# Performance work log

Measured on AMD Instinct MI355X. Metric: run time of the kernel, lower is better.

## Reference

```python
import jax, jax.numpy as jnp
import numpy as np

MARGIN = 1.0
EPS = 1e-8  # torch F.cosine_similarity default eps


def setup_inputs() -> dict:
    key = jax.random.key(0)
    k1, k2 = jax.random.split(key)
    reps = jax.random.normal(k1, (8192, 512), dtype=jnp.float32)
    labels = jax.random.randint(k2, (8192,), 0, 100, dtype=jnp.int64)
    return {"reps": reps, "labels": labels}


def reference(reps, labels):
    # cosine_similarity(reps[None, :, :], reps[:, None, :], dim=2)
    # == dot(a,b) / (max(||a||,eps) * max(||b||,eps)); compute via normalize + GEMM
    norms = jnp.maximum(jnp.linalg.norm(reps, axis=1, keepdims=True), EPS)
    xn = reps / norms  # [N, D]
    cos_sim = xn @ xn.T  # [N, N]
    label_matrix = labels[None, :] == labels[:, None]  # [N, N] bool
    same_class_loss = jnp.where(label_matrix, (1.0 - cos_sim) ** 2, 0.0)
    diff_class_loss = jnp.where(label_matrix, 0.0,
                                jnp.maximum(MARGIN - cos_sim, 0.0) ** 2)
    loss = same_class_loss + diff_class_loss
    return loss.mean()
```

## Files before the change

kernel.cpp:

```cpp
#include <hip/hip_runtime.h>


typedef __attribute__((ext_vector_type(8))) short  s8;
typedef __attribute__((ext_vector_type(8))) __bf16 bf8;
typedef __attribute__((ext_vector_type(4))) float  f4;
typedef __attribute__((ext_vector_type(4))) unsigned short u4v;

#define NTILE 36
#define PS_F32 (NTILE * 4096)

#define OFF_XT  0u
#define OFF_INV (8u * 1024u * 1024u)
#define OFF_S   (OFF_INV + 8192u * 4u)
#define OFF_S2  (OFF_S + 512u * 4u)
#define OFF_GP  (8u * 1024u * 1024u + 65536u)

__device__ __forceinline__ unsigned short f2bf(float f) {
    union { float f; unsigned u; } v; v.f = f;
    unsigned r = v.u + 0x7FFFu + ((v.u >> 16) & 1u);
    return (unsigned short)(r >> 16);
}

__global__ __launch_bounds__(256) void k_norms(
    const float* __restrict__ reps, float* __restrict__ inv,
    float* __restrict__ zbuf )
{
    const int t = threadIdx.x, lane = t & 63, w = t >> 6;
    if (blockIdx.x == 0) {
        for (int z = t; z < 513; z += 256) zbuf[z] = 0.f;
    }
    const int row = blockIdx.x * 4 + w;
    const float4 x0 = *(const float4*)(reps + (size_t)row * 512 + lane * 4);
    const float4 x1 = *(const float4*)(reps + (size_t)row * 512 + 256 + lane * 4);
    float ss = x0.x*x0.x + x0.y*x0.y + x0.z*x0.z + x0.w*x0.w
             + x1.x*x1.x + x1.y*x1.y + x1.z*x1.z + x1.w*x1.w;
    #pragma unroll
    for (int off = 1; off < 64; off <<= 1) ss += __shfl_xor(ss, off, 64);
    if (lane == 0) inv[row] = 1.0f / fmaxf(sqrtf(ss), 1e-8f);
}

__global__ __launch_bounds__(256) void k_norm_transpose(
    const float* __restrict__ reps, const float* __restrict__ inv,
    unsigned short* __restrict__ xt, float* __restrict__ svec)
{
    __shared__ unsigned short tile[64][72];
    __shared__ float sred[4][64];
    const int t = threadIdx.x, lane = t & 63, w = t >> 6;
    const int a0 = blockIdx.x * 64, i0 = blockIdx.y * 64;
    const int colg = t & 15;
    const int ig0  = t >> 4;

    float4 sa = {0.f, 0.f, 0.f, 0.f};
    #pragma unroll
    for (int j = 0; j < 4; ++j) {
        const int il = ig0 + j * 16;
        const float iv = inv[i0 + il];
        const float4 x = *(const float4*)(reps + (size_t)(i0 + il) * 512 + a0 + colg * 4);
        const float4 xn = {x.x * iv, x.y * iv, x.z * iv, x.w * iv};
        sa.x += xn.x; sa.y += xn.y; sa.z += xn.z; sa.w += xn.w;
        ushort4 p;
        p.x = f2bf(xn.x); p.y = f2bf(xn.y); p.z = f2bf(xn.z); p.w = f2bf(xn.w);
        *(ushort4*)&tile[il][colg * 4] = p;
    }
    __syncthreads();

    {
        const int ig = t & 15, ag = t >> 4;
        u4v rows[4];
        #pragma unroll
        for (int r = 0; r < 4; ++r)
            rows[r] = *(const u4v*)&tile[ig * 4 + r][ag * 4];
        #pragma unroll
        for (int j = 0; j < 4; ++j) {
            ushort4 o;
            o.x = (unsigned short)rows[0][j];
            o.y = (unsigned short)rows[1][j];
            o.z = (unsigned short)rows[2][j];
            o.w = (unsigned short)rows[3][j];
            *(ushort4*)(xt + (size_t)(a0 + ag * 4 + j) * 8192 + i0 + ig * 4) = o;
        }
    }

    sa.x += __shfl_xor(sa.x, 16, 64); sa.x += __shfl_xor(sa.x, 32, 64);
    sa.y += __shfl_xor(sa.y, 16, 64); sa.y += __shfl_xor(sa.y, 32, 64);
    sa.z += __shfl_xor(sa.z, 16, 64); sa.z += __shfl_xor(sa.z, 32, 64);
    sa.w += __shfl_xor(sa.w, 16, 64); sa.w += __shfl_xor(sa.w, 32, 64);
    if (lane < 16) {
        sred[w][lane * 4 + 0] = sa.x; sred[w][lane * 4 + 1] = sa.y;
        sred[w][lane * 4 + 2] = sa.z; sred[w][lane * 4 + 3] = sa.w;
    }
    __syncthreads();
    if (t < 64) {
        const float v = sred[0][t] + sred[1][t] + sred[2][t] + sred[3][t];
        atomicAdd(&svec[a0 + t], v);
    }
}

__global__ __launch_bounds__(64) void k_gram(
    const unsigned short* __restrict__ xt, float* __restrict__ gp, int kc)
{
    const int lane = threadIdx.x;
    const int l15 = lane & 15, l4 = lane >> 4;
    int tt = blockIdx.x, ta = 0;
    while (tt >= 8 - ta) { tt -= 8 - ta; ++ta; }
    const int tb = ta + tt;
    const int a0 = ta * 64, b0 = tb * 64;
    const int k0 = blockIdx.z * kc;
    const unsigned short* Arow = xt + (size_t)(a0 + l15) * 8192;
    const unsigned short* Brow = xt + (size_t)(b0 + l15) * 8192;

    f4 acc[4][4];
    #pragma unroll
    for (int mi = 0; mi < 4; ++mi)
        #pragma unroll
        for (int ni = 0; ni < 4; ++ni) {
            f4 z = {0.f, 0.f, 0.f, 0.f};
            acc[mi][ni] = z;
        }

    for (int k = 0; k < kc; k += 32) {
        const int ko = k0 + k + l4 * 8;
        s8 af[4], bfr[4];
        #pragma unroll
        for (int mi = 0; mi < 4; ++mi)
            af[mi] = *(const s8*)(Arow + (size_t)mi * 16 * 8192 + ko);
        #pragma unroll
        for (int ni = 0; ni < 4; ++ni)
            bfr[ni] = *(const s8*)(Brow + (size_t)ni * 16 * 8192 + ko);
        #pragma unroll
        for (int mi = 0; mi < 4; ++mi)
            #pragma unroll
            for (int ni = 0; ni < 4; ++ni)
                acc[mi][ni] = __builtin_amdgcn_mfma_f32_16x16x32_bf16(
                    __builtin_bit_cast(bf8, af[mi]),
                    __builtin_bit_cast(bf8, bfr[ni]),
                    acc[mi][ni], 0, 0, 0);
    }

    float* gb = gp + (size_t)blockIdx.z * PS_F32 + (size_t)blockIdx.x * 4096;
    #pragma unroll
    for (int mi = 0; mi < 4; ++mi)
        #pragma unroll
        for (int ni = 0; ni < 4; ++ni)
            #pragma unroll
            for (int r = 0; r < 4; ++r) {
                const int a_ = mi * 16 + l4 * 4 + r;
                const int b_ = ni * 16 + l15;
                gb[a_ * 64 + b_] = acc[mi][ni][r];
            }
}

__global__ __launch_bounds__(256) void k_reduce(
    const float* __restrict__ gp, float* __restrict__ s2, int ksplit)
{
    const int c = blockIdx.x * 256 + threadIdx.x;
    const f4* g4 = (const f4*)gp;
    f4 s = {0.f, 0.f, 0.f, 0.f};
    for (int p = 0; p < ksplit; ++p) s += g4[(size_t)p * (PS_F32 / 4) + c];
    int tt = c >> 10, ta = 0;
    while (tt >= 8 - ta) { tt -= 8 - ta; ++ta; }
    const float wgt = (tt == 0) ? 1.f : 2.f;
    float sq = wgt * (s.x * s.x + s.y * s.y + s.z * s.z + s.w * s.w);
    #pragma unroll
    for (int off = 1; off < 64; off <<= 1) sq += __shfl_xor(sq, off, 64);
    __shared__ float part[4];
    if ((threadIdx.x & 63) == 0) part[threadIdx.x >> 6] = sq;
    __syncthreads();
    if (threadIdx.x == 0) atomicAdd(s2, part[0] + part[1] + part[2] + part[3]);
}

__global__ __launch_bounds__(512) void k_final(
    const float* __restrict__ svec, const float* __restrict__ s2,
    float* __restrict__ out)
{
    const int t = threadIdx.x;
    float v = svec[t];
    float p = v * v;
    #pragma unroll
    for (int off = 1; off < 64; off <<= 1) p += __shfl_xor(p, off, 64);
    __shared__ float part[8];
    if ((t & 63) == 0) part[t >> 6] = p;
    __syncthreads();
    if (t == 0) {
        float s1 = 0.f;
        #pragma unroll
        for (int q = 0; q < 8; ++q) s1 += part[q];
        const double NN = 67108864.0;
        double loss = (NN - 2.0 * (double)s1 + (double)(*s2)) / NN;
        out[0] = (float)loss;
    }
}

extern "C" void kernel_launch(void* const* d_in, const int* in_sizes, int n_in,
                              void* d_out, int out_size, void* d_ws, size_t ws_size,
                              hipStream_t stream)
{
    const float* reps = (const float*)d_in[0];
    char* ws = (char*)d_ws;
    unsigned short* xt   = (unsigned short*)(ws + OFF_XT);
    float*          invn = (float*)(ws + OFF_INV);
    float*          svec = (float*)(ws + OFF_S);
    float*          s2   = (float*)(ws + OFF_S2);
    float*          gp   = (float*)(ws + OFF_GP);

    const size_t psb = (size_t)PS_F32 * 4;
    int ksplit = 8;
    if (ws_size >= OFF_GP + 32 * psb)      ksplit = 32;
    else if (ws_size >= OFF_GP + 16 * psb) ksplit = 16;
    const int kc = 8192 / ksplit;

    k_norms<<<2048, 256, 0, stream>>>(reps, invn, svec);
    k_norm_transpose<<<dim3(8, 128), 256, 0, stream>>>(reps, invn, xt, svec);
    k_gram<<<dim3(NTILE, 1, ksplit), 64, 0, stream>>>(xt, gp, kc);
    k_reduce<<<144, 256, 0, stream>>>(gp, s2, ksplit);
    k_final<<<1, 512, 0, stream>>>(svec, s2, (float*)d_out);
}
```

Baseline: 97.45 us.

## Use 32x32 Gram tiles with fixed K-split and fuse reduce with final

The upper-triangle tiling of the 512x512 Gram matrix moves from 64x64 tiles (36 tiles) to 32x32 tiles (136 tiles), with a fixed split of K=8192 into 16 chunks. This gives more workgroups to fill the GPU's compute units and removes the workspace-size-dependent split. The separate final kernel is folded into the reduction kernel through an atomic ticket, so the last block computes the loss and one launch is saved. In exchange, each tile reuses its loaded operands less, fewer rows per block share each fragment load, and the ticket counter must be zeroed (it is added to the zeroing range).

```diff
diff --git a/kernel.cpp b/kernel.cpp
--- a/kernel.cpp
+++ b/kernel.cpp
@@ -6,14 +6,16 @@
 typedef __attribute__((ext_vector_type(4))) float  f4;
 typedef __attribute__((ext_vector_type(4))) unsigned short u4v;
 
-#define NTILE 36
-#define PS_F32 (NTILE * 4096)
+#define NT32 136
+#define KOUT 16
+#define KCW  512
 
 #define OFF_XT  0u
 #define OFF_INV (8u * 1024u * 1024u)
 #define OFF_S   (OFF_INV + 8192u * 4u)
 #define OFF_S2  (OFF_S + 512u * 4u)
-#define OFF_GP  (8u * 1024u * 1024u + 65536u)
+#define OFF_TK  (OFF_S2 + 4u)
+#define OFF_GP  (OFF_S2 + 64u)
 
 __device__ __forceinline__ unsigned short f2bf(float f) {
     union { float f; unsigned u; } v; v.f = f;
@@ -27,7 +29,7 @@
 {
     const int t = threadIdx.x, lane = t & 63, w = t >> 6;
     if (blockIdx.x == 0) {
-        for (int z = t; z < 513; z += 256) zbuf[z] = 0.f;
+        for (int z = t; z < 514; z += 256) zbuf[z] = 0.f;
     }
     const int row = blockIdx.x * 4 + w;
     const float4 x0 = *(const float4*)(reps + (size_t)row * 512 + lane * 4);
@@ -97,97 +99,97 @@
 }
 
 __global__ __launch_bounds__(64) void k_gram(
-    const unsigned short* __restrict__ xt, float* __restrict__ gp, int kc)
+    const unsigned short* __restrict__ xt, float* __restrict__ gp)
 {
     const int lane = threadIdx.x;
     const int l15 = lane & 15, l4 = lane >> 4;
     int tt = blockIdx.x, ta = 0;
-    while (tt >= 8 - ta) { tt -= 8 - ta; ++ta; }
+    while (tt >= 16 - ta) { tt -= 16 - ta; ++ta; }
     const int tb = ta + tt;
-    const int a0 = ta * 64, b0 = tb * 64;
-    const int k0 = blockIdx.z * kc;
-    const unsigned short* Arow = xt + (size_t)(a0 + l15) * 8192;
-    const unsigned short* Brow = xt + (size_t)(b0 + l15) * 8192;
-
-    f4 acc[4][4];
-    #pragma unroll
-    for (int mi = 0; mi < 4; ++mi)
-        #pragma unroll
-        for (int ni = 0; ni < 4; ++ni) {
+    const int k0 = blockIdx.y * KCW;
+    const unsigned short* Arow = xt + (size_t)(ta * 32 + l15) * 8192;
+    const unsigned short* Brow = xt + (size_t)(tb * 32 + l15) * 8192;
+
+    f4 acc[2][2];
+    #pragma unroll
+    for (int mi = 0; mi < 2; ++mi)
+        #pragma unroll
+        for (int ni = 0; ni < 2; ++ni) {
             f4 z = {0.f, 0.f, 0.f, 0.f};
             acc[mi][ni] = z;
         }
 
-    for (int k = 0; k < kc; k += 32) {
+    for (int k = 0; k < KCW; k += 32) {
         const int ko = k0 + k + l4 * 8;
-        s8 af[4], bfr[4];
-        #pragma unroll
-        for (int mi = 0; mi < 4; ++mi)
-            af[mi] = *(const s8*)(Arow + (size_t)mi * 16 * 8192 + ko);
-        #pragma unroll
-        for (int ni = 0; ni < 4; ++ni)
-            bfr[ni] = *(const s8*)(Brow + (size_t)ni * 16 * 8192 + ko);
-        #pragma unroll
-        for (int mi = 0; mi < 4; ++mi)
+        s8 af[2], bfr[2];
+        af[0]  = *(const s8*)(Arow + ko);
+        af[1]  = *(const s8*)(Arow + (size_t)16 * 8192 + ko);
+        bfr[0] = *(const s8*)(Brow + ko);
+        bfr[1] = *(const s8*)(Brow + (size_t)16 * 8192 + ko);
+        #pragma unroll
+        for (int mi = 0; mi < 2; ++mi)
             #pragma unroll
-            for (int ni = 0; ni < 4; ++ni)
+            for (int ni = 0; ni < 2; ++ni)
                 acc[mi][ni] = __builtin_amdgcn_mfma_f32_16x16x32_bf16(
                     __builtin_bit_cast(bf8, af[mi]),
                     __builtin_bit_cast(bf8, bfr[ni]),
                     acc[mi][ni], 0, 0, 0);
     }
 
-    float* gb = gp + (size_t)blockIdx.z * PS_F32 + (size_t)blockIdx.x * 4096;
-    #pragma unroll
-    for (int mi = 0; mi < 4; ++mi)
-        #pragma unroll
-        for (int ni = 0; ni < 4; ++ni)
+    float* gb = gp + ((size_t)blockIdx.y * NT32 + blockIdx.x) * 1024;
+    #pragma unroll
+    for (int mi = 0; mi < 2; ++mi)
+        #pragma unroll
+        for (int ni = 0; ni < 2; ++ni)
             #pragma unroll
             for (int r = 0; r < 4; ++r) {
                 const int a_ = mi * 16 + l4 * 4 + r;
                 const int b_ = ni * 16 + l15;
-                gb[a_ * 64 + b_] = acc[mi][ni][r];
+                gb[a_ * 32 + b_] = acc[mi][ni][r];
             }
 }
 
-__global__ __launch_bounds__(256) void k_reduce(
-    const float* __restrict__ gp, float* __restrict__ s2, int ksplit)
-{
-    const int c = blockIdx.x * 256 + threadIdx.x;
+__global__ __launch_bounds__(256) void k_reduce_final(
+    const float* __restrict__ gp, const float* __restrict__ svec,
+    float* __restrict__ s2, int* __restrict__ ticket,
+    float* __restrict__ out)
+{
+    __shared__ float part[4];
+    __shared__ int lastFlag;
+    const int t = threadIdx.x;
+    const int c = blockIdx.x * 256 + t;
     const f4* g4 = (const f4*)gp;
     f4 s = {0.f, 0.f, 0.f, 0.f};
-    for (int p = 0; p < ksplit; ++p) s += g4[(size_t)p * (PS_F32 / 4) + c];
-    int tt = c >> 10, ta = 0;
-    while (tt >= 8 - ta) { tt -= 8 - ta; ++ta; }
+    #pragma unroll
+    for (int p = 0; p < KOUT; ++p) s += g4[(size_t)p * (NT32 * 256) + c];
+    int tt = c >> 8, ta = 0;
+    while (tt >= 16 - ta) { tt -= 16 - ta; ++ta; }
     const float wgt = (tt == 0) ? 1.f : 2.f;
     float sq = wgt * (s.x * s.x + s.y * s.y + s.z * s.z + s.w * s.w);
     #pragma unroll
     for (int off = 1; off < 64; off <<= 1) sq += __shfl_xor(sq, off, 64);
-    __shared__ float part[4];
-    if ((threadIdx.x & 63) == 0) part[threadIdx.x >> 6] = sq;
-    __syncthreads();
-    if (threadIdx.x == 0) atomicAdd(s2, part[0] + part[1] + part[2] + part[3]);
-}
-
-__global__ __launch_bounds__(512) void k_final(
-    const float* __restrict__ svec, const float* __restrict__ s2,
-    float* __restrict__ out)
-{
-    const int t = threadIdx.x;
-    float v = svec[t];
-    float p = v * v;
-    #pragma unroll
-    for (int off = 1; off < 64; off <<= 1) p += __shfl_xor(p, off, 64);
-    __shared__ float part[8];
-    if ((t & 63) == 0) part[t >> 6] = p;
+    if ((t & 63) == 0) part[t >> 6] = sq;
     __syncthreads();
     if (t == 0) {
-        float s1 = 0.f;
-        #pragma unroll
-        for (int q = 0; q < 8; ++q) s1 += part[q];
-        const double NN = 67108864.0;
-        double loss = (NN - 2.0 * (double)s1 + (double)(*s2)) / NN;
-        out[0] = (float)loss;
+        atomicAdd(s2, part[0] + part[1] + part[2] + part[3]);
+        __threadfence();
+        lastFlag = (atomicAdd(ticket, 1) == (int)gridDim.x - 1);
+    }
+    __syncthreads();
+    if (lastFlag) {
+        __threadfence();
+        const float v0 = svec[t], v1 = svec[t + 256];
+        float p = v0 * v0 + v1 * v1;
+        #pragma unroll
+        for (int off = 1; off < 64; off <<= 1) p += __shfl_xor(p, off, 64);
+        if ((t & 63) == 0) part[t >> 6] = p;
+        __syncthreads();
+        if (t == 0) {
+            const float s1 = part[0] + part[1] + part[2] + part[3];
+            const float S2 = atomicAdd(s2, 0.f);
+            const double NN = 67108864.0;
+            out[0] = (float)((NN - 2.0 * (double)s1 + (double)S2) / NN);
+        }
     }
 }
 
@@ -201,17 +203,11 @@
     float*          invn = (float*)(ws + OFF_INV);
     float*          svec = (float*)(ws + OFF_S);
     float*          s2   = (float*)(ws + OFF_S2);
+    int*            tick = (int*)(ws + OFF_TK);
     float*          gp   = (float*)(ws + OFF_GP);
-
-    const size_t psb = (size_t)PS_F32 * 4;
-    int ksplit = 8;
-    if (ws_size >= OFF_GP + 32 * psb)      ksplit = 32;
-    else if (ws_size >= OFF_GP + 16 * psb) ksplit = 16;
-    const int kc = 8192 / ksplit;
 
     k_norms<<<2048, 256, 0, stream>>>(reps, invn, svec);
     k_norm_transpose<<<dim3(8, 128), 256, 0, stream>>>(reps, invn, xt, svec);
-    k_gram<<<dim3(NTILE, 1, ksplit), 64, 0, stream>>>(xt, gp, kc);
-    k_reduce<<<144, 256, 0, stream>>>(gp, s2, ksplit);
-    k_final<<<1, 512, 0, stream>>>(svec, s2, (float*)d_out);
-}
+    k_gram<<<dim3(NT32, KOUT), 64, 0, stream>>>(xt, gp);
+    k_reduce_final<<<NT32, 256, 0, stream>>>(gp, svec, s2, tick, (float*)d_out);
+}
```

Result: no change. 98.70 us (+1.3%).
